# Optimization experiments

Hardware: AMD Instinct MI355X
Metric: run time of the kernel (lower is better)

## Reference

```python
import jax, jax.numpy as jnp
import numpy as np

B, L, D = 2, 2048, 1024   # batch, seq, hidden_dim (= hidden_dim_)
H = 8                      # heads (hardcoded in module)


def setup_inputs() -> dict:
    key = jax.random.key(0)
    ks = jax.random.split(key, 12)
    std = float(np.sqrt(2.0 / D))
    inp = {
        "en": jax.random.normal(ks[0], (B, L, D), jnp.float32),
        "de": jax.random.normal(ks[1], (B, L, D), jnp.float32),
        "mask": jax.random.randint(ks[2], (B, L, L), 0, 2).astype(bool),
        # Linear weights stored as (in, out) so that y = x @ W + b
        "Wq": jax.random.normal(ks[3], (D, D), jnp.float32) * std,
        "bq": jnp.zeros((D,), jnp.float32),
        "Wk": jax.random.normal(ks[4], (D, D), jnp.float32) * std,
        "bk": jnp.zeros((D,), jnp.float32),
        "Wv": jax.random.normal(ks[5], (D, D), jnp.float32) * std,
        "bv": jnp.zeros((D,), jnp.float32),
        "Wo": jax.random.normal(ks[6], (D, D), jnp.float32) * float(np.sqrt(2.0 / (2 * D))),
        "bo": jnp.zeros((D,), jnp.float32),
        "gamma": jnp.float32(1.0),
        "beta": jnp.float32(0.0),
    }
    return inp


def reference(en, de, mask, Wq, bq, Wk, bk, Wv, bv, Wo, bo, gamma, beta):
    b, lq, d_model = de.shape
    lk = en.shape[1]
    d_k = float(d_model)  # module uses de.shape[-1], i.e. full hidden dim
    # faithful head split: view(B,L,-1,8) -> head index is the LAST axis
    q = (de @ Wq + bq).reshape(b, lq, -1, H).transpose(3, 0, 1, 2)   # (H,B,Lq,hd)
    k = (en @ Wk + bk).reshape(b, lk, -1, H).transpose(3, 0, 3 - 1, 1)[...] if False else (en @ Wk + bk).reshape(b, lk, -1, H).transpose(3, 0, 2, 1)  # (H,B,hd,Lk)
    v = (en @ Wv + bv).reshape(b, lk, -1, H).transpose(3, 0, 1, 2)   # (H,B,Lk,hd)
    e = jnp.matmul(q, k) / np.sqrt(d_k)                               # (H,B,Lq,Lk)
    e = jnp.where(mask, jnp.float32(-1e10), e)
    alpha = jax.nn.softmax(e, axis=-1)
    head3 = jnp.matmul(alpha, v)                                      # (H,B,Lq,hd)
    # torch.cat((head3[0],...,head3[7]), dim=2) == move head axis before hd and flatten
    a = jnp.transpose(head3, (1, 2, 0, 3)).reshape(b, lq, -1)         # (B,Lq,H*hd)
    result = a @ Wo + bo + de                                         # residual BEFORE Norm
    mu = jnp.mean(result, axis=2, keepdims=True)
    var = jnp.var(result, axis=2, ddof=1, keepdims=True)              # torch.var unbiased=True
    out = gamma * (result - mu) / jnp.sqrt(var + 1e-8) + beta
    return out
```

## Files before the change

### kernel.cpp

```cpp
#include <hip/hip_runtime.h>
#include <hip/hip_bf16.h>

#define D_MODEL 1024
#define SEQ     2048
#define BATCH   2
#define NH      8
#define HD      128
#define MTOT    4096

typedef __attribute__((ext_vector_type(4))) float f32x4;
typedef __attribute__((ext_vector_type(8))) short bf16x8;

#define BF_XDE 0u
#define BF_XEN 4194304u
#define BF_WQT 8388608u
#define BF_WKT 9437184u
#define BF_WVT 10485760u
#define BF_WOT 11534336u
#define BF_QB  12582912u
#define BF_KB  16777216u
#define BF_VT  20971520u
#define BF_AB  25165824u

__device__ __forceinline__ float4 ldg4(const float* p) {
  return *reinterpret_cast<const float4*>(p);
}

__device__ __forceinline__ void load_lds16(const void* g, void* l) {
  __builtin_amdgcn_global_load_lds((const __attribute__((address_space(1))) void*)g,
                                   (__attribute__((address_space(3))) void*)l, 16, 0, 0);
}

__global__ __launch_bounds__(256) void castx_kernel(const float* __restrict__ de,
                                                    const float* __restrict__ en,
                                                    __hip_bfloat16* __restrict__ Xde,
                                                    __hip_bfloat16* __restrict__ Xen) {
  const float* src = blockIdx.y ? en : de;
  __hip_bfloat16* dst = blockIdx.y ? Xen : Xde;
  const size_t base = (size_t)blockIdx.x * 4096 + (size_t)threadIdx.x * 16;
  float tmp[16];
#pragma unroll
  for (int i = 0; i < 4; ++i) {
    const float4 v = ldg4(src + base + i * 4);
    tmp[i * 4 + 0] = v.x; tmp[i * 4 + 1] = v.y; tmp[i * 4 + 2] = v.z; tmp[i * 4 + 3] = v.w;
  }
  __hip_bfloat16 ob[16];
#pragma unroll
  for (int i = 0; i < 16; ++i) ob[i] = __float2bfloat16(tmp[i]);
  *reinterpret_cast<uint4*>(dst + base)     = *reinterpret_cast<const uint4*>(ob);
  *reinterpret_cast<uint4*>(dst + base + 8) = *reinterpret_cast<const uint4*>(ob + 8);
}

__global__ __launch_bounds__(256) void castw_kernel(const float* __restrict__ Wq,
                                                    const float* __restrict__ Wk,
                                                    const float* __restrict__ Wv,
                                                    const float* __restrict__ Wo,
                                                    __hip_bfloat16* __restrict__ WtBase) {
  __shared__ __hip_bfloat16 tile[64][68];
  const int z = blockIdx.z;
  const float* W = (z == 0) ? Wq : (z == 1) ? Wk : (z == 2) ? Wv : Wo;
  __hip_bfloat16* Wt = WtBase + (size_t)z * 1048576;
  const int n0 = blockIdx.x * 64, k0 = blockIdx.y * 64;
  const int t = threadIdx.x;
#pragma unroll
  for (int i = 0; i < 4; ++i) {
    const int kr = (t >> 4) + i * 16, cg = t & 15;
    const float4 v = ldg4(W + (size_t)(k0 + kr) * D_MODEL + n0 + cg * 4);
    __hip_bfloat16 tb[4] = {__float2bfloat16(v.x), __float2bfloat16(v.y),
                            __float2bfloat16(v.z), __float2bfloat16(v.w)};
    *reinterpret_cast<ushort4*>(&tile[kr][cg * 4]) = *reinterpret_cast<const ushort4*>(tb);
  }
  __syncthreads();
  const int nr = t >> 2, ks = (t & 3) * 16;
  __hip_bfloat16 ob[16];
#pragma unroll
  for (int j = 0; j < 16; ++j) ob[j] = tile[ks + j][nr];
  __hip_bfloat16* dst = Wt + (size_t)(n0 + nr) * D_MODEL + k0 + ks;
  *reinterpret_cast<uint4*>(dst)     = *reinterpret_cast<const uint4*>(ob);
  *reinterpret_cast<uint4*>(dst + 8) = *reinterpret_cast<const uint4*>(ob + 8);
}

__device__ __forceinline__ void mfma_core(const __hip_bfloat16* __restrict__ Ag,
                                          const __hip_bfloat16* __restrict__ Bg,
                                          int m0, int n0,
                                          __hip_bfloat16* Asm, __hip_bfloat16* Bsm,
                                          f32x4 acc[4][4]) {
  const int t = threadIdx.x, w = t >> 6, l = t & 63;
  const int lr = l & 15, lg = l >> 4;
  const int wr = w >> 1, wc = w & 1;
  const int lrow = l >> 3;
  const int lcol = (l & 7) * 8;

#pragma unroll
  for (int a = 0; a < 4; ++a)
#pragma unroll
    for (int b = 0; b < 4; ++b) acc[a][b] = (f32x4){0.f, 0.f, 0.f, 0.f};

  for (int ks = 0; ks < D_MODEL / 64; ++ks) {
    __syncthreads();
#pragma unroll
    for (int j = 0; j < 4; ++j) {
      const int chunk = w * 4 + j;
      const int row = chunk * 8 + lrow;
      load_lds16(Ag + (size_t)(m0 + row) * D_MODEL + ks * 64 + lcol, Asm + chunk * 512);
      load_lds16(Bg + (size_t)(n0 + row) * D_MODEL + ks * 64 + lcol, Bsm + chunk * 512);
    }
    __syncthreads();
#pragma unroll
    for (int kk = 0; kk < 2; ++kk) {
      bf16x8 af[4], bf[4];
#pragma unroll
      for (int fm = 0; fm < 4; ++fm)
        af[fm] = *reinterpret_cast<const bf16x8*>(Asm + (wr * 64 + fm * 16 + lr) * 64 + kk * 32 + lg * 8);
#pragma unroll
      for (int fn = 0; fn < 4; ++fn)
        bf[fn] = *reinterpret_cast<const bf16x8*>(Bsm + (wc * 64 + fn * 16 + lr) * 64 + kk * 32 + lg * 8);
#pragma unroll
      for (int fm = 0; fm < 4; ++fm)
#pragma unroll
        for (int fn = 0; fn < 4; ++fn)
          acc[fm][fn] = __builtin_amdgcn_mfma_f32_16x16x32_bf16(af[fm], bf[fn], acc[fm][fn], 0, 0, 0);
    }
  }
}

__global__ __launch_bounds__(256, 2) void gemm_qkv_kernel(
    const __hip_bfloat16* __restrict__ Xde, const __hip_bfloat16* __restrict__ Xen,
    const __hip_bfloat16* __restrict__ WtQ,
    const float* __restrict__ bq, const float* __restrict__ bk, const float* __restrict__ bv,
    __hip_bfloat16* __restrict__ Qb, __hip_bfloat16* __restrict__ Kb,
    __hip_bfloat16* __restrict__ Vt) {
  __shared__ __hip_bfloat16 Asm[128 * 64];
  __shared__ __hip_bfloat16 Bsm[128 * 64];
  const int z = blockIdx.z;
  const __hip_bfloat16* Ag = (z == 0) ? Xde : Xen;
  const __hip_bfloat16* Bg = WtQ + (size_t)z * 1048576;
  const float* bias = (z == 0) ? bq : (z == 1) ? bk : bv;
  const int m0 = blockIdx.y * 128, n0 = blockIdx.x * 128;
  f32x4 acc[4][4];
  mfma_core(Ag, Bg, m0, n0, Asm, Bsm, acc);

  const int t = threadIdx.x, w = t >> 6, l = t & 63;
  const int lr = l & 15, lg = l >> 4, wr = w >> 1, wc = w & 1;
#pragma unroll
  for (int fn = 0; fn < 4; ++fn) {
    const int n = n0 + wc * 64 + fn * 16 + lr;
    const float bve = bias[n];
    const int h = n & 7, c = n >> 3;
#pragma unroll
    for (int fm = 0; fm < 4; ++fm)
#pragma unroll
      for (int i = 0; i < 4; ++i) {
        const int m = m0 + wr * 64 + fm * 16 + lg * 4 + i;
        const int b = m >> 11, ll = m & 2047;
        const __hip_bfloat16 v = __float2bfloat16(acc[fm][fn][i] + bve);
        if (z == 2) Vt[((size_t)(b * NH + h) * HD + c) * SEQ + ll] = v;
        else {
          __hip_bfloat16* dst = (z == 0) ? Qb : Kb;
          dst[((size_t)(b * NH + h) * SEQ + ll) * HD + c] = v;
        }
      }
  }
}

__global__ __launch_bounds__(256, 2) void gemm_out_kernel(
    const __hip_bfloat16* __restrict__ Ab, const __hip_bfloat16* __restrict__ Wot,
    const float* __restrict__ bo, const float* __restrict__ de,
    float* __restrict__ R) {
  __shared__ __hip_bfloat16 Asm[128 * 64];
  __shared__ __hip_bfloat16 Bsm[128 * 64];
  const int m0 = blockIdx.y * 128, n0 = blockIdx.x * 128;
  f32x4 acc[4][4];
  mfma_core(Ab, Wot, m0, n0, Asm, Bsm, acc);

  const int t = threadIdx.x, w = t >> 6, l = t & 63;
  const int lr = l & 15, lg = l >> 4, wr = w >> 1, wc = w & 1;
#pragma unroll
  for (int fn = 0; fn < 4; ++fn) {
    const int n = n0 + wc * 64 + fn * 16 + lr;
    const float bve = bo[n];
#pragma unroll
    for (int fm = 0; fm < 4; ++fm)
#pragma unroll
      for (int i = 0; i < 4; ++i) {
        const int m = m0 + wr * 64 + fm * 16 + lg * 4 + i;
        R[(size_t)m * D_MODEL + n] = acc[fm][fn][i] + bve + de[(size_t)m * D_MODEL + n];
      }
  }
}

__global__ __launch_bounds__(256, 2) void attn_kernel(const __hip_bfloat16* __restrict__ Qb,
                                                      const __hip_bfloat16* __restrict__ Kb,
                                                      const __hip_bfloat16* __restrict__ Vtb,
                                                      const int* __restrict__ mask,
                                                      __hip_bfloat16* __restrict__ Ab) {
  __shared__ __hip_bfloat16 Qs[64][136];
  __shared__ __hip_bfloat16 Ks[64][136];
  __shared__ __hip_bfloat16 Vt[128][72];
  __shared__ __hip_bfloat16 Ps[64][72];

  const int qb = blockIdx.x, bh = blockIdx.y;
  const int b = bh >> 3, h = bh & 7;
  const int t = threadIdx.x;
  const int w = t >> 6, l = t & 63;
  const int lr = l & 15, lg = l >> 4;
  const int q0 = qb * 64;

  const __hip_bfloat16* Qg = Qb + (size_t)bh * SEQ * HD;
  const __hip_bfloat16* Kg = Kb + (size_t)bh * SEQ * HD;
  const __hip_bfloat16* Vg = Vtb + (size_t)bh * HD * SEQ;

#pragma unroll
  for (int it = 0; it < 4; ++it) {
    const int idx = t + it * 256;
    const int r = idx >> 4, cc = idx & 15;
    *reinterpret_cast<uint4*>(&Qs[r][cc * 8]) =
        *reinterpret_cast<const uint4*>(Qg + (size_t)(q0 + r) * HD + cc * 8);
  }

  float m_run[4], l_run[4];
  f32x4 o[8];
#pragma unroll
  for (int i = 0; i < 4; ++i) { m_run[i] = -INFINITY; l_run[i] = 0.f; }
#pragma unroll
  for (int dt = 0; dt < 8; ++dt) o[dt] = (f32x4){0.f, 0.f, 0.f, 0.f};

  for (int kt = 0; kt < SEQ / 64; ++kt) {
    const int k0 = kt * 64;
    __syncthreads();
#pragma unroll
    for (int it = 0; it < 4; ++it) {
      const int idx = t + it * 256;
      const int r = idx >> 4, cc = idx & 15;
      *reinterpret_cast<uint4*>(&Ks[r][cc * 8]) =
          *reinterpret_cast<const uint4*>(Kg + (size_t)(k0 + r) * HD + cc * 8);
      const int d = idx >> 3, ck = idx & 7;
      *reinterpret_cast<uint4*>(&Vt[d][ck * 8]) =
          *reinterpret_cast<const uint4*>(Vg + (size_t)d * SEQ + k0 + ck * 8);
    }
    __syncthreads();

    f32x4 s[4];
#pragma unroll
    for (int nt = 0; nt < 4; ++nt) s[nt] = (f32x4){0.f, 0.f, 0.f, 0.f};
#pragma unroll
    for (int kc = 0; kc < 4; ++kc) {
      const bf16x8 afr = *reinterpret_cast<const bf16x8*>(&Qs[w * 16 + lr][kc * 32 + lg * 8]);
#pragma unroll
      for (int nt = 0; nt < 4; ++nt) {
        const bf16x8 bfr = *reinterpret_cast<const bf16x8*>(&Ks[nt * 16 + lr][kc * 32 + lg * 8]);
        s[nt] = __builtin_amdgcn_mfma_f32_16x16x32_bf16(afr, bfr, s[nt], 0, 0, 0);
      }
    }

    const int* mbase = mask + ((size_t)b * SEQ + q0 + w * 16 + lg * 4) * SEQ + k0 + lr;
    float p[4][4];
#pragma unroll
    for (int i = 0; i < 4; ++i) {
      const int* mrow = mbase + (size_t)i * SEQ;
      float v0 = mrow[0]  ? -1e10f : s[0][i] * 0.03125f;
      float v1 = mrow[16] ? -1e10f : s[1][i] * 0.03125f;
      float v2 = mrow[32] ? -1e10f : s[2][i] * 0.03125f;
      float v3 = mrow[48] ? -1e10f : s[3][i] * 0.03125f;
      p[0][i] = v0; p[1][i] = v1; p[2][i] = v2; p[3][i] = v3;

      float rm = fmaxf(fmaxf(v0, v1), fmaxf(v2, v3));
      rm = fmaxf(rm, __shfl_xor(rm, 1, 64));
      rm = fmaxf(rm, __shfl_xor(rm, 2, 64));
      rm = fmaxf(rm, __shfl_xor(rm, 4, 64));
      rm = fmaxf(rm, __shfl_xor(rm, 8, 64));
      const float mn = fmaxf(m_run[i], rm);
      const float sf = __expf(m_run[i] - mn);
      m_run[i] = mn;
      float rs = 0.f;
#pragma unroll
      for (int nt = 0; nt < 4; ++nt) {
        const float pe = __expf(p[nt][i] - mn);
        p[nt][i] = pe;
        rs += pe;
      }
      rs += __shfl_xor(rs, 1, 64);
      rs += __shfl_xor(rs, 2, 64);
      rs += __shfl_xor(rs, 4, 64);
      rs += __shfl_xor(rs, 8, 64);
      l_run[i] = l_run[i] * sf + rs;
#pragma unroll
      for (int dt = 0; dt < 8; ++dt) o[dt][i] *= sf;
#pragma unroll
      for (int nt = 0; nt < 4; ++nt)
        Ps[w * 16 + lg * 4 + i][nt * 16 + lr] = __float2bfloat16(p[nt][i]);
    }

#pragma unroll
    for (int ksb = 0; ksb < 2; ++ksb) {
      const bf16x8 pa = *reinterpret_cast<const bf16x8*>(&Ps[w * 16 + lr][ksb * 32 + lg * 8]);
#pragma unroll
      for (int dt = 0; dt < 8; ++dt) {
        const bf16x8 vb = *reinterpret_cast<const bf16x8*>(&Vt[dt * 16 + lr][ksb * 32 + lg * 8]);
        o[dt] = __builtin_amdgcn_mfma_f32_16x16x32_bf16(pa, vb, o[dt], 0, 0, 0);
      }
    }
  }

  __hip_bfloat16* Abp = Ab + ((size_t)b * SEQ + q0 + w * 16 + lg * 4) * D_MODEL + h * HD + lr;
#pragma unroll
  for (int i = 0; i < 4; ++i) {
    const float inv = 1.f / l_run[i];
#pragma unroll
    for (int dt = 0; dt < 8; ++dt)
      Abp[(size_t)i * D_MODEL + dt * 16] = __float2bfloat16(o[dt][i] * inv);
  }
}

__global__ __launch_bounds__(256) void ln_kernel(const float* __restrict__ R,
                                                 const float* __restrict__ gptr,
                                                 const float* __restrict__ bptr,
                                                 float* __restrict__ out) {
  __shared__ float red[8];
  const int m = blockIdx.x, t = threadIdx.x;
  const int lane = t & 63, wid = t >> 6;
  const float4 x = ldg4(R + (size_t)m * D_MODEL + t * 4);
  float s = x.x + x.y + x.z + x.w;
#pragma unroll
  for (int off = 1; off < 64; off <<= 1) s += __shfl_xor(s, off, 64);
  if (lane == 0) red[wid] = s;
  __syncthreads();
  const float mu = (red[0] + red[1] + red[2] + red[3]) * (1.f / 1024.f);
  const float dx = x.x - mu, dy = x.y - mu, dz = x.z - mu, dw = x.w - mu;
  float sq = dx * dx + dy * dy + dz * dz + dw * dw;
#pragma unroll
  for (int off = 1; off < 64; off <<= 1) sq += __shfl_xor(sq, off, 64);
  if (lane == 0) red[4 + wid] = sq;
  __syncthreads();
  const float var = (red[4] + red[5] + red[6] + red[7]) * (1.f / 1023.f);
  const float inv = rsqrtf(var + 1e-8f);
  const float g = gptr[0], be = bptr[0];
  float4 ov;
  ov.x = g * dx * inv + be;
  ov.y = g * dy * inv + be;
  ov.z = g * dz * inv + be;
  ov.w = g * dw * inv + be;
  *reinterpret_cast<float4*>(&out[(size_t)m * D_MODEL + t * 4]) = ov;
}

extern "C" void kernel_launch(void* const* d_in, const int* in_sizes, int n_in,
                              void* d_out, int out_size, void* d_ws, size_t ws_size,
                              hipStream_t stream) {
  const float* en   = (const float*)d_in[0];
  const float* de   = (const float*)d_in[1];
  const int*   mask = (const int*)d_in[2];
  const float* Wq   = (const float*)d_in[3];
  const float* bq   = (const float*)d_in[4];
  const float* Wk   = (const float*)d_in[5];
  const float* bk   = (const float*)d_in[6];
  const float* Wv   = (const float*)d_in[7];
  const float* bv   = (const float*)d_in[8];
  const float* Wo   = (const float*)d_in[9];
  const float* bo   = (const float*)d_in[10];
  const float* gamma = (const float*)d_in[11];
  const float* beta  = (const float*)d_in[12];
  float* ws  = (float*)d_ws;
  float* out = (float*)d_out;

  float* R = ws;
  __hip_bfloat16* bfb = (__hip_bfloat16*)(ws + 4194304);
  __hip_bfloat16* Xde = bfb + BF_XDE;
  __hip_bfloat16* Xen = bfb + BF_XEN;
  __hip_bfloat16* Wqt = bfb + BF_WQT;
  __hip_bfloat16* Wot = bfb + BF_WOT;
  __hip_bfloat16* Qb  = bfb + BF_QB;
  __hip_bfloat16* Kb  = bfb + BF_KB;
  __hip_bfloat16* Vt  = bfb + BF_VT;
  __hip_bfloat16* Ab  = bfb + BF_AB;

  castx_kernel<<<dim3(1024, 2), 256, 0, stream>>>(de, en, Xde, Xen);
  castw_kernel<<<dim3(16, 16, 4), 256, 0, stream>>>(Wq, Wk, Wv, Wo, Wqt);
  gemm_qkv_kernel<<<dim3(8, 32, 3), 256, 0, stream>>>(Xde, Xen, Wqt, bq, bk, bv, Qb, Kb, Vt);
  attn_kernel<<<dim3(32, 16), 256, 0, stream>>>(Qb, Kb, Vt, mask, Ab);
  gemm_out_kernel<<<dim3(8, 32), 256, 0, stream>>>(Ab, Wot, bo, de, R);
  ln_kernel<<<MTOT, 256, 0, stream>>>(R, gamma, beta, out);
}
```

Before: 339.2 us.

## Bit-pack mask, prefetch K/V into registers, stage QKV epilogue through LDS

A new pre-pass packs the int32 mask into 64-bit ballot words, so the attention kernel reads one word per row per tile instead of sixteen scattered ints. The attention kernel now keeps Q fragments in registers, prefetches the next K/V tile into registers while the current one is computed, raises wave priority around the MFMA blocks, and targets 3 waves per SIMD. The QKV GEMM epilogue now transposes through shared memory, replacing strided scalar stores with coalesced 16-byte stores. The trade-offs are an extra kernel launch and workspace buffer for the packed mask, plus higher register pressure from the prefetch buffers.

```diff
diff --git a/kernel.cpp b/kernel.cpp
--- a/kernel.cpp
+++ b/kernel.cpp
@@ -14,13 +14,12 @@
 #define BF_XDE 0u
 #define BF_XEN 4194304u
 #define BF_WQT 8388608u
-#define BF_WKT 9437184u
-#define BF_WVT 10485760u
 #define BF_WOT 11534336u
 #define BF_QB  12582912u
 #define BF_KB  16777216u
 #define BF_VT  20971520u
 #define BF_AB  25165824u
+#define BF_MB  29360128u
 
 __device__ __forceinline__ float4 ldg4(const float* p) {
   return *reinterpret_cast<const float4*>(p);
@@ -29,6 +28,24 @@
 __device__ __forceinline__ void load_lds16(const void* g, void* l) {
   __builtin_amdgcn_global_load_lds((const __attribute__((address_space(1))) void*)g,
                                    (__attribute__((address_space(3))) void*)l, 16, 0, 0);
+}
+
+__device__ __forceinline__ void barrier_lgkm() {
+  asm volatile("s_waitcnt lgkmcnt(0)" ::: "memory");
+  __builtin_amdgcn_s_barrier();
+}
+
+__global__ __launch_bounds__(256) void mask_pack_kernel(const int* __restrict__ mask,
+                                                        unsigned long long* __restrict__ Mb) {
+  const int lane = threadIdx.x & 63;
+  const int gw = blockIdx.x * 4 + (threadIdx.x >> 6);
+  const int nw = gridDim.x * 4;
+  const int nwords = (BATCH * SEQ * SEQ) / 64;
+  for (int w = gw; w < nwords; w += nw) {
+    const int v = mask[(size_t)w * 64 + lane];
+    const unsigned long long bits = __ballot(v != 0);
+    if (lane == 0) Mb[w] = bits;
+  }
 }
 
 __global__ __launch_bounds__(256) void castx_kernel(const float* __restrict__ de,
@@ -130,36 +147,62 @@
     const float* __restrict__ bq, const float* __restrict__ bk, const float* __restrict__ bv,
     __hip_bfloat16* __restrict__ Qb, __hip_bfloat16* __restrict__ Kb,
     __hip_bfloat16* __restrict__ Vt) {
-  __shared__ __hip_bfloat16 Asm[128 * 64];
-  __shared__ __hip_bfloat16 Bsm[128 * 64];
+  __shared__ __hip_bfloat16 smem[16896];
   const int z = blockIdx.z;
   const __hip_bfloat16* Ag = (z == 0) ? Xde : Xen;
   const __hip_bfloat16* Bg = WtQ + (size_t)z * 1048576;
   const float* bias = (z == 0) ? bq : (z == 1) ? bk : bv;
   const int m0 = blockIdx.y * 128, n0 = blockIdx.x * 128;
   f32x4 acc[4][4];
-  mfma_core(Ag, Bg, m0, n0, Asm, Bsm, acc);
+  mfma_core(Ag, Bg, m0, n0, smem, smem + 8192, acc);
 
   const int t = threadIdx.x, w = t >> 6, l = t & 63;
   const int lr = l & 15, lg = l >> 4, wr = w >> 1, wc = w & 1;
+
+  __syncthreads();
+  __hip_bfloat16 (*Ct)[132] = reinterpret_cast<__hip_bfloat16(*)[132]>(smem);
 #pragma unroll
   for (int fn = 0; fn < 4; ++fn) {
-    const int n = n0 + wc * 64 + fn * 16 + lr;
-    const float bve = bias[n];
-    const int h = n & 7, c = n >> 3;
-#pragma unroll
-    for (int fm = 0; fm < 4; ++fm)
-#pragma unroll
-      for (int i = 0; i < 4; ++i) {
-        const int m = m0 + wr * 64 + fm * 16 + lg * 4 + i;
-        const int b = m >> 11, ll = m & 2047;
-        const __hip_bfloat16 v = __float2bfloat16(acc[fm][fn][i] + bve);
-        if (z == 2) Vt[((size_t)(b * NH + h) * HD + c) * SEQ + ll] = v;
-        else {
-          __hip_bfloat16* dst = (z == 0) ? Qb : Kb;
-          dst[((size_t)(b * NH + h) * SEQ + ll) * HD + c] = v;
-        }
-      }
+    const int nl = wc * 64 + fn * 16 + lr;
+    const float bve = bias[n0 + nl];
+#pragma unroll
+    for (int fm = 0; fm < 4; ++fm) {
+      const int ml = wr * 64 + fm * 16 + lg * 4;
+#pragma unroll
+      for (int i = 0; i < 4; ++i)
+        Ct[ml + i][nl] = __float2bfloat16(acc[fm][fn][i] + bve);
+    }
+  }
+  __syncthreads();
+
+  const int b = m0 >> 11, l0 = m0 & 2047, c0 = n0 >> 3;
+  if (z != 2) {
+    __hip_bfloat16* dst = (z == 0) ? Qb : Kb;
+#pragma unroll
+    for (int j = 0; j < 8; ++j) {
+      const int cid = t + j * 256;
+      const int hh = cid >> 8, ll = (cid >> 1) & 127, half = cid & 1;
+      __hip_bfloat16 ob[8];
+#pragma unroll
+      for (int cc = 0; cc < 8; ++cc)
+        ob[cc] = Ct[ll][(half * 8 + cc) * 8 + hh];
+      *reinterpret_cast<uint4*>(dst + ((size_t)(b * NH + hh) * SEQ + l0 + ll) * HD + c0 + half * 8) =
+          *reinterpret_cast<const uint4*>(ob);
+    }
+  } else {
+#pragma unroll
+    for (int j = 0; j < 8; ++j) {
+      const int cid = t + j * 256;
+      const int nl = cid >> 4, chunk = cid & 15;
+      const int n = n0 + nl;
+      const int hh = n & 7, c = n >> 3;
+      __hip_bfloat16 ob[8];
+#pragma unroll
+      for (int cc = 0; cc < 8; ++cc)
+        ob[cc] = Ct[chunk * 8 + cc][nl];
+      *reinterpret_cast<uint4*>(Vt + ((size_t)(b * NH + hh) * HD + c) * SEQ + l0 + chunk * 8) =
+          *reinterpret_cast<const uint4*>(ob);
+    }
   }
 }
 
@@ -189,12 +232,11 @@
   }
 }
 
-__global__ __launch_bounds__(256, 2) void attn_kernel(const __hip_bfloat16* __restrict__ Qb,
+__global__ __launch_bounds__(256, 3) void attn_kernel(const __hip_bfloat16* __restrict__ Qb,
                                                       const __hip_bfloat16* __restrict__ Kb,
                                                       const __hip_bfloat16* __restrict__ Vtb,
-                                                      const int* __restrict__ mask,
+                                                      const unsigned long long* __restrict__ Mb,
                                                       __hip_bfloat16* __restrict__ Ab) {
-  __shared__ __hip_bfloat16 Qs[64][136];
   __shared__ __hip_bfloat16 Ks[64][136];
   __shared__ __hip_bfloat16 Vt[128][72];
   __shared__ __hip_bfloat16 Ps[64][72];
@@ -210,13 +252,24 @@
   const __hip_bfloat16* Kg = Kb + (size_t)bh * SEQ * HD;
   const __hip_bfloat16* Vg = Vtb + (size_t)bh * HD * SEQ;
 
-#pragma unroll
-  for (int it = 0; it < 4; ++it) {
-    const int idx = t + it * 256;
-    const int r = idx >> 4, cc = idx & 15;
-    *reinterpret_cast<uint4*>(&Qs[r][cc * 8]) =
-        *reinterpret_cast<const uint4*>(Qg + (size_t)(q0 + r) * HD + cc * 8);
-  }
+  bf16x8 qf[4];
+#pragma unroll
+  for (int kc = 0; kc < 4; ++kc)
+    qf[kc] = *reinterpret_cast<const bf16x8*>(Qg + (size_t)(q0 + w * 16 + lr) * HD + kc * 32 + lg * 8);
+
+  uint4 kreg[4], vreg[4];
+  auto prefetch = [&](int kt) {
+    const int k0 = kt * 64;
+#pragma unroll
+    for (int it = 0; it < 4; ++it) {
+      const int idx = t + it * 256;
+      kreg[it] = *reinterpret_cast<const uint4*>(Kg + (size_t)(k0 + (idx >> 4)) * HD + (idx & 15) * 8);
+      vreg[it] = *reinterpret_cast<const uint4*>(Vg + (size_t)(idx >> 3) * SEQ + k0 + (idx & 7) * 8);
+    }
+  };
+  prefetch(0);
+
+  const unsigned long long* Mrow = Mb + ((size_t)b * SEQ + q0 + w * 16 + lg * 4) * 32;
 
   float m_run[4], l_run[4];
   f32x4 o[8];
@@ -226,42 +279,41 @@
   for (int dt = 0; dt < 8; ++dt) o[dt] = (f32x4){0.f, 0.f, 0.f, 0.f};
 
   for (int kt = 0; kt < SEQ / 64; ++kt) {
-    const int k0 = kt * 64;
-    __syncthreads();
+    barrier_lgkm();
 #pragma unroll
     for (int it = 0; it < 4; ++it) {
       const int idx = t + it * 256;
-      const int r = idx >> 4, cc = idx & 15;
-      *reinterpret_cast<uint4*>(&Ks[r][cc * 8]) =
-          *reinterpret_cast<const uint4*>(Kg + (size_t)(k0 + r) * HD + cc * 8);
-      const int d = idx >> 3, ck = idx & 7;
-      *reinterpret_cast<uint4*>(&Vt[d][ck * 8]) =
-          *reinterpret_cast<const uint4*>(Vg + (size_t)d * SEQ + k0 + ck * 8);
-    }
-    __syncthreads();
+      *reinterpret_cast<uint4*>(&Ks[idx >> 4][(idx & 15) * 8]) = kreg[it];
+      *reinterpret_cast<uint4*>(&Vt[idx >> 3][(idx & 7) * 8]) = vreg[it];
+    }
+    unsigned long long mw[4];
+#pragma unroll
+    for (int i = 0; i < 4; ++i) mw[i] = Mrow[(size_t)i * 32 + kt];
+    if (kt + 1 < SEQ / 64) prefetch(kt + 1);
+    barrier_lgkm();
 
     f32x4 s[4];
 #pragma unroll
     for (int nt = 0; nt < 4; ++nt) s[nt] = (f32x4){0.f, 0.f, 0.f, 0.f};
+    __builtin_amdgcn_s_setprio(1);
 #pragma unroll
     for (int kc = 0; kc < 4; ++kc) {
-      const bf16x8 afr = *reinterpret_cast<const bf16x8*>(&Qs[w * 16 + lr][kc * 32 + lg * 8]);
 #pragma unroll
       for (int nt = 0; nt < 4; ++nt) {
         const bf16x8 bfr = *reinterpret_cast<const bf16x8*>(&Ks[nt * 16 + lr][kc * 32 + lg * 8]);
-        s[nt] = __builtin_amdgcn_mfma_f32_16x16x32_bf16(afr, bfr, s[nt], 0, 0, 0);
+        s[nt] = __builtin_amdgcn_mfma_f32_16x16x32_bf16(qf[kc], bfr, s[nt], 0, 0, 0);
       }
     }
-
-    const int* mbase = mask + ((size_t)b * SEQ + q0 + w * 16 + lg * 4) * SEQ + k0 + lr;
+    __builtin_amdgcn_s_setprio(0);
+
     float p[4][4];
 #pragma unroll
     for (int i = 0; i < 4; ++i) {
-      const int* mrow = mbase + (size_t)i * SEQ;
-      float v0 = mrow[0]  ? -1e10f : s[0][i] * 0.03125f;
-      float v1 = mrow[16] ? -1e10f : s[1][i] * 0.03125f;
-      float v2 = mrow[32] ? -1e10f : s[2][i] * 0.03125f;
-      float v3 = mrow[48] ? -1e10f : s[3][i] * 0.03125f;
+      const unsigned long long mwi = mw[i];
+      float v0 = ((mwi >> (lr))      & 1ull) ? -1e10f : s[0][i] * 0.03125f;
+      float v1 = ((mwi >> (16 + lr)) & 1ull) ? -1e10f : s[1][i] * 0.03125f;
+      float v2 = ((mwi >> (32 + lr)) & 1ull) ? -1e10f : s[2][i] * 0.03125f;
+      float v3 = ((mwi >> (48 + lr)) & 1ull) ? -1e10f : s[3][i] * 0.03125f;
       p[0][i] = v0; p[1][i] = v1; p[2][i] = v2; p[3][i] = v3;
 
       float rm = fmaxf(fmaxf(v0, v1), fmaxf(v2, v3));
@@ -291,6 +343,7 @@
         Ps[w * 16 + lg * 4 + i][nt * 16 + lr] = __float2bfloat16(p[nt][i]);
     }
 
+    __builtin_amdgcn_s_setprio(1);
 #pragma unroll
     for (int ksb = 0; ksb < 2; ++ksb) {
       const bf16x8 pa = *reinterpret_cast<const bf16x8*>(&Ps[w * 16 + lr][ksb * 32 + lg * 8]);
@@ -300,6 +353,7 @@
         o[dt] = __builtin_amdgcn_mfma_f32_16x16x32_bf16(pa, vb, o[dt], 0, 0, 0);
       }
     }
+    __builtin_amdgcn_s_setprio(0);
   }
 
   __hip_bfloat16* Abp = Ab + ((size_t)b * SEQ + q0 + w * 16 + lg * 4) * D_MODEL + h * HD + lr;
@@ -372,11 +426,13 @@
   __hip_bfloat16* Kb  = bfb + BF_KB;
   __hip_bfloat16* Vt  = bfb + BF_VT;
   __hip_bfloat16* Ab  = bfb + BF_AB;
+  unsigned long long* Mb = (unsigned long long*)(bfb + BF_MB);
 
   castx_kernel<<<dim3(1024, 2), 256, 0, stream>>>(de, en, Xde, Xen);
   castw_kernel<<<dim3(16, 16, 4), 256, 0, stream>>>(Wq, Wk, Wv, Wo, Wqt);
+  mask_pack_kernel<<<1024, 256, 0, stream>>>(mask, Mb);
   gemm_qkv_kernel<<<dim3(8, 32, 3), 256, 0, stream>>>(Xde, Xen, Wqt, bq, bk, bv, Qb, Kb, Vt);
-  attn_kernel<<<dim3(32, 16), 256, 0, stream>>>(Qb, Kb, Vt, mask, Ab);
+  attn_kernel<<<dim3(32, 16), 256, 0, stream>>>(Qb, Kb, Vt, Mb, Ab);
   gemm_out_kernel<<<dim3(8, 32), 256, 0, stream>>>(Ab, Wot, bo, de, R);
   ln_kernel<<<MTOT, 256, 0, stream>>>(R, gamma, beta, out);
 }
```

Result: slower. 446.5 us (+31.6%).
